# Kernel optimization log

Measured on AMD Instinct MI355X. Metric: run time of the kernel, lower is better.

## Reference

```python
import jax, jax.numpy as jnp
import numpy as np
import math

H, D = 8, 16
O = H * D  # out_channels = 128
N_TYPES = 2
EDGE_META = [(0, 1), (1, 0)]  # (src_type, dst_type) per edge type: user->item, item->user

def _segment_softmax(alpha, dst, n):
    # PyG softmax over incoming edges grouped by destination node
    amax = jax.ops.segment_max(alpha, dst, num_segments=n)
    amax = jnp.where(jnp.isfinite(amax), amax, 0.0)
    ex = jnp.exp(alpha - amax[dst])
    den = jax.ops.segment_sum(ex, dst, num_segments=n)
    return ex / (den[dst] + 1e-16)

def setup_inputs():
    key = jax.random.key(0)
    ks = jax.random.split(key, 8)
    N, E, I = 50000, 500000, 128
    s = 1.0 / math.sqrt(I)
    sd = 1.0 / math.sqrt(D)
    return {
        "x": jax.random.normal(ks[0], (N_TYPES, N, I), jnp.float32),
        "k_w": jax.random.normal(ks[1], (N_TYPES, O, I), jnp.float32) * s,
        "k_b": jnp.zeros((N_TYPES, O), jnp.float32),
        "q_w": jax.random.normal(ks[2], (N_TYPES, O, I), jnp.float32) * s,
        "q_b": jnp.zeros((N_TYPES, O), jnp.float32),
        "v_w": jax.random.normal(ks[3], (N_TYPES, O, I), jnp.float32) * s,
        "v_b": jnp.zeros((N_TYPES, O), jnp.float32),
        "a_w": jax.random.normal(ks[4], (N_TYPES, O, O), jnp.float32) * s,
        "a_b": jnp.zeros((N_TYPES, O), jnp.float32),
        "skip": jnp.ones((N_TYPES,), jnp.float32),
        "a_rel": jax.random.normal(ks[5], (2, H, D, D), jnp.float32) * sd,
        "m_rel": jax.random.normal(ks[6], (2, H, D, D), jnp.float32) * sd,
        "p_rel": jnp.ones((2, H), jnp.float32),
        "ln_g": jnp.ones((O,), jnp.float32),
        "ln_b": jnp.zeros((O,), jnp.float32),
        "edge_index": jax.random.randint(ks[7], (2, 2, E), 0, N, jnp.int32),
    }

def reference(x, k_w, k_b, q_w, q_b, v_w, v_b, a_w, a_b, skip, a_rel, m_rel, p_rel, ln_g, ln_b, edge_index):
    N = x.shape[1]
    lin = lambda xi, w, b: xi @ w.T + b
    # per-node-type K/Q/V projections -> [T, N, H, D]
    k = jnp.stack([lin(x[t], k_w[t], k_b[t]) for t in range(N_TYPES)]).reshape(N_TYPES, N, H, D)
    q = jnp.stack([lin(x[t], q_w[t], q_b[t]) for t in range(N_TYPES)]).reshape(N_TYPES, N, H, D)
    v = jnp.stack([lin(x[t], v_w[t], v_b[t]) for t in range(N_TYPES)]).reshape(N_TYPES, N, H, D)
    agg = jnp.zeros((N_TYPES, N, O), x.dtype)
    for e, (st, dt) in enumerate(EDGE_META):
        src, dst = edge_index[e, 0], edge_index[e, 1]
        ke = jnp.einsum('nhd,hde->nhe', k[st], a_rel[e])  # relation-transformed keys
        ve = jnp.einsum('nhd,hde->nhe', v[st], m_rel[e])  # relation-transformed values
        alpha = jnp.einsum('ehd,ehd->eh', q[dt][dst], ke[src]) * p_rel[e] / math.sqrt(D)
        alpha = _segment_softmax(alpha, dst, N)  # [E, H]
        msg = (ve[src] * alpha[..., None]).reshape(-1, O)
        agg = agg.at[dt].add(jax.ops.segment_sum(msg, dst, num_segments=N))
    outs = []
    for t in range(N_TYPES):
        o = lin(jax.nn.gelu(agg[t], approximate=False), a_w[t], a_b[t])
        beta = jax.nn.sigmoid(skip[t])
        o = beta * o + (1.0 - beta) * x[t]  # HGT skip (out_channels == in_channels)
        o = jax.nn.relu(o)
        mu = jnp.mean(o, axis=-1, keepdims=True)
        var = jnp.mean((o - mu) ** 2, axis=-1, keepdims=True)
        o = (o - mu) / jnp.sqrt(var + 1e-5) * ln_g + ln_b  # LayerNorm; dropout = identity (eval)
        outs.append(o)
    return jnp.stack(outs)  # [2, N, 128]
```

## Files before the change

kernel.cpp:

```cpp
#include <hip/hip_runtime.h>
#include <math.h>


#define EB_STRIDE 40

typedef __attribute__((ext_vector_type(8))) short short8;
typedef __attribute__((ext_vector_type(4))) float floatx4;

__device__ __forceinline__ float bf2f(unsigned int bits16) {
  union { unsigned int i; float f; } u; u.i = bits16 << 16; return u.f;
}
__device__ __forceinline__ float bf2f_hi(unsigned int u) {
  union { unsigned int i; float f; } v; v.i = u & 0xffff0000u; return v.f;
}
__device__ __forceinline__ unsigned short f2bf(float f) {
  union { float ff; unsigned int i; } u; u.ff = f;
  unsigned int x = u.i;
  x += 0x7fffu + ((x >> 16) & 1u);
  return (unsigned short)(x >> 16);
}

__global__ void fuse_weights(
    const float* __restrict__ k_w, const float* __restrict__ k_b,
    const float* __restrict__ q_w, const float* __restrict__ q_b,
    const float* __restrict__ v_w, const float* __restrict__ v_b,
    const float* __restrict__ a_w, const float* __restrict__ a_b,
    const float* __restrict__ a_rel, const float* __restrict__ m_rel,
    const float* __restrict__ p_rel,
    unsigned short* __restrict__ Wfb, float* __restrict__ Bf,
    int* __restrict__ cnt, int nC)
{
  int tid = blockIdx.x * 256 + threadIdx.x;
  if (tid < nC) cnt[tid] = 0;
  if (tid >= 2 * 4 * 128 * 128) return;
  int t   = tid >> 16;
  int rem = tid & 65535;
  int m   = rem >> 14;
  int o   = (rem >> 7) & 127;
  int i   = rem & 127;
  float w, bias;
  if (m == 0) {
    w    = q_w[t * 16384 + o * 128 + i];
    bias = q_b[t * 128 + o];
  } else if (m == 3) {
    w    = a_w[t * 16384 + o * 128 + i];
    bias = a_b[t * 128 + o];
  } else {
    const float* bw  = (m == 1) ? k_w : v_w;
    const float* bb  = (m == 1) ? k_b : v_b;
    const float* rel = (m == 1) ? a_rel : m_rel;
    int h = o >> 4, eo = o & 15;
    float s = 0.f, sb = 0.f;
    #pragma unroll
    for (int d = 0; d < 16; ++d) {
      float r = rel[t * 2048 + h * 256 + d * 16 + eo];
      s  += bw[t * 16384 + (h * 16 + d) * 128 + i] * r;
      sb += bb[t * 128 + h * 16 + d] * r;
    }
    if (m == 1) {
      float sc = p_rel[t * 8 + h] * 0.25f;
      s *= sc; sb *= sc;
    }
    w = s; bias = sb;
  }
  Wfb[tid] = f2bf(w);
  if (i == 0) Bf[t * 512 + m * 128 + o] = bias;
}

__global__ __launch_bounds__(256) void qkv_fill(
    const float* __restrict__ x, const unsigned short* __restrict__ Wfb,
    const float* __restrict__ Bf, unsigned short* __restrict__ qbuf,
    unsigned short* __restrict__ kvbuf,
    const int* __restrict__ ei, int* __restrict__ cnt, int* __restrict__ ebuf,
    int Nn, int E, int Gg)
{
  __shared__ alignas(16) unsigned short Als[64][136];
  __shared__ alignas(16) unsigned short Bls[128][136];
  const int b = blockIdx.x;
  const int tid = threadIdx.x;

  if (b >= Gg) {
    int f = b - Gg;
    int e = f & 1;
    int i = (f >> 1) * 256 + tid;
    if (i < E) {
      int src = ei[(size_t)e * 2 * E + i];
      int dst = ei[(size_t)e * 2 * E + E + i];
      int bk = (1 - e) * Nn + dst;
      int pos = atomicAdd(&cnt[bk], 1);
      if (pos < EB_STRIDE) ebuf[(size_t)bk * EB_STRIDE + pos] = src;
    }
    return;
  }

  const int t = b & 1;
  const int m0 = (b >> 1) * 64;
  const int lane = tid & 63, w = tid >> 6;
  const int col = lane & 15, quad = lane >> 4;
  const int morder[3] = {1, 2, 0};

  {
    int r = tid & 63, h = tid >> 6;
    int gn = m0 + r;
    if (gn < Nn) {
      const float* ap = x + (size_t)t * Nn * 128 + (size_t)gn * 128 + h * 32;
      #pragma unroll
      for (int j = 0; j < 8; ++j) {
        float4 f = ((const float4*)ap)[j];
        ushort4 s;
        s.x = f2bf(f.x); s.y = f2bf(f.y); s.z = f2bf(f.z); s.w = f2bf(f.w);
        *(ushort4*)&Als[r][h * 32 + j * 4] = s;
      }
    } else {
      ushort4 z = make_ushort4(0, 0, 0, 0);
      #pragma unroll
      for (int j = 0; j < 8; ++j) *(ushort4*)&Als[r][h * 32 + j * 4] = z;
    }
  }

  float acc_k[8][4];
  float bias_n[8];

  for (int mi_ = 0; mi_ < 3; ++mi_) {
    int m = morder[mi_];
    __syncthreads();
    {
      int r = tid & 127, h = tid >> 7;
      const unsigned short* wp = Wfb + (((size_t)(t * 4 + m)) << 14) + r * 128 + h * 64;
      #pragma unroll
      for (int j = 0; j < 8; ++j)
        *(uint4*)&Bls[r][h * 64 + j * 8] = ((const uint4*)wp)[j];
    }
    __syncthreads();

    floatx4 acc[8];
    #pragma unroll
    for (int ni = 0; ni < 8; ++ni) acc[ni] = (floatx4)(0.f);

    #pragma unroll
    for (int k0 = 0; k0 < 128; k0 += 32) {
      int kk = k0 + quad * 8;
      short8 a0 = *(const short8*)&Als[w * 16 + col][kk];
      #pragma unroll
      for (int ni = 0; ni < 8; ++ni) {
        short8 bb = *(const short8*)&Bls[ni * 16 + col][kk];
        acc[ni] = __builtin_amdgcn_mfma_f32_16x16x32_bf16(a0, bb, acc[ni], 0, 0, 0);
      }
    }

    const float* Bv = Bf + t * 512 + m * 128;
    #pragma unroll
    for (int ni = 0; ni < 8; ++ni) bias_n[ni] = Bv[ni * 16 + col];

    if (m == 1) {
      #pragma unroll
      for (int ni = 0; ni < 8; ++ni)
        #pragma unroll
        for (int reg = 0; reg < 4; ++reg)
          acc_k[ni][reg] = acc[ni][reg] + bias_n[ni];
    } else if (m == 2) {
      unsigned int* kvp = (unsigned int*)kvbuf + ((size_t)t * Nn) * 128;
      #pragma unroll
      for (int reg = 0; reg < 4; ++reg) {
        int row = m0 + w * 16 + quad * 4 + reg;
        if (row >= Nn) continue;
        unsigned int* cp = kvp + (size_t)row * 128 + col;
        #pragma unroll
        for (int ni = 0; ni < 8; ++ni) {
          unsigned int kbits = f2bf(acc_k[ni][reg]);
          unsigned int vbits = f2bf(acc[ni][reg] + bias_n[ni]);
          cp[ni * 16] = (vbits << 16) | kbits;
        }
      }
    } else {
      #pragma unroll
      for (int reg = 0; reg < 4; ++reg) {
        int row = m0 + w * 16 + quad * 4 + reg;
        if (row >= Nn) continue;
        unsigned short* cp = qbuf + ((size_t)t * Nn + row) * 128 + col;
        #pragma unroll
        for (int ni = 0; ni < 8; ++ni)
          cp[ni * 16] = f2bf(acc[ni][reg] + bias_n[ni]);
      }
    }
  }
}

__global__ __launch_bounds__(256) void gather_fused(
    const unsigned short* __restrict__ qbuf, const unsigned short* __restrict__ kvbuf,
    const int* __restrict__ cnt, const int* __restrict__ ebuf,
    unsigned short* __restrict__ gbuf, int N)
{
  int wid = (blockIdx.x * 256 + threadIdx.x) >> 6;
  int l = threadIdx.x & 63;
  if (wid >= 2 * N) return;
  int dt = (wid >= N) ? 1 : 0;
  int e  = 1 - dt;
  int deg = cnt[wid]; if (deg > EB_STRIDE) deg = EB_STRIDE;
  int g = l >> 4, gl = l & 15;

  uint4 qr = *(const uint4*)(qbuf + (size_t)wid * 128 + 8 * gl);
  float qv[8];
  qv[0] = bf2f(qr.x & 0xffffu); qv[1] = bf2f(qr.x >> 16);
  qv[2] = bf2f(qr.y & 0xffffu); qv[3] = bf2f(qr.y >> 16);
  qv[4] = bf2f(qr.z & 0xffffu); qv[5] = bf2f(qr.z >> 16);
  qv[6] = bf2f(qr.w & 0xffffu); qv[7] = bf2f(qr.w >> 16);

  const unsigned short* kvbase = kvbuf + ((size_t)e * N) * 256;
  const int* eb = ebuf + (size_t)wid * EB_STRIDE;
  int mysrc = (l < deg) ? eb[l] : 0;

  float acc[8];
  #pragma unroll
  for (int c = 0; c < 8; ++c) acc[c] = 0.f;
  float den = 0.f;

  for (int j0 = 0; j0 < deg; j0 += 4) {
    int j = j0 + g;
    bool valid = j < deg;
    int src = __shfl(mysrc, valid ? j : 0, 64);
    const unsigned short* kv = kvbase + (size_t)src * 256 + 16 * gl;
    uint4 a = *(const uint4*)kv;
    uint4 b = *(const uint4*)(kv + 8);
    float p;
    p = qv[0] * bf2f(a.x & 0xffffu);
    p = fmaf(qv[1], bf2f(a.y & 0xffffu), p);
    p = fmaf(qv[2], bf2f(a.z & 0xffffu), p);
    p = fmaf(qv[3], bf2f(a.w & 0xffffu), p);
    p = fmaf(qv[4], bf2f(b.x & 0xffffu), p);
    p = fmaf(qv[5], bf2f(b.y & 0xffffu), p);
    p = fmaf(qv[6], bf2f(b.z & 0xffffu), p);
    p = fmaf(qv[7], bf2f(b.w & 0xffffu), p);
    float pt = p + __shfl_xor(p, 1, 64);
    float ex = valid ? __expf(pt) : 0.f;
    den += ex;
    acc[0] = fmaf(ex, bf2f_hi(a.x), acc[0]);
    acc[1] = fmaf(ex, bf2f_hi(a.y), acc[1]);
    acc[2] = fmaf(ex, bf2f_hi(a.z), acc[2]);
    acc[3] = fmaf(ex, bf2f_hi(a.w), acc[3]);
    acc[4] = fmaf(ex, bf2f_hi(b.x), acc[4]);
    acc[5] = fmaf(ex, bf2f_hi(b.y), acc[5]);
    acc[6] = fmaf(ex, bf2f_hi(b.z), acc[6]);
    acc[7] = fmaf(ex, bf2f_hi(b.w), acc[7]);
  }

  #pragma unroll
  for (int off = 16; off < 64; off <<= 1) {
    #pragma unroll
    for (int c = 0; c < 8; ++c) acc[c] += __shfl_xor(acc[c], off, 64);
    den += __shfl_xor(den, off, 64);
  }

  if (g == 0) {
    float rden = 1.f / (den + 1e-16f);
    unsigned short r[8];
    #pragma unroll
    for (int c = 0; c < 8; ++c) {
      float gg = acc[c] * rden;
      r[c] = f2bf(0.5f * gg * (1.f + erff(gg * 0.70710678118654752f)));
    }
    unsigned short* op = gbuf + (size_t)wid * 128 + 8 * gl;
    *(ushort4*)op       = make_ushort4(r[0], r[1], r[2], r[3]);
    *(ushort4*)(op + 4) = make_ushort4(r[4], r[5], r[6], r[7]);
  }
}

__global__ __launch_bounds__(256) void gemm_ln(
    const unsigned short* __restrict__ gbuf, const unsigned short* __restrict__ Wfb,
    const float* __restrict__ Bf, const float* __restrict__ x,
    const float* __restrict__ skip, const float* __restrict__ ln_g,
    const float* __restrict__ ln_b, float* __restrict__ outp, int Nn)
{
  __shared__ alignas(16) unsigned short Als[64][136];
  __shared__ alignas(16) unsigned short Bls[128][136];
  const int tid = threadIdx.x;
  const int t = blockIdx.x & 1;
  const int m0 = (blockIdx.x >> 1) * 64;
  const int lane = tid & 63, w = tid >> 6;
  const int col = lane & 15, quad = lane >> 4;

  {
    int r = tid & 63, h = tid >> 6;
    int gn = m0 + r;
    if (gn < Nn) {
      const unsigned short* ap = gbuf + (size_t)t * Nn * 128 + (size_t)gn * 128 + h * 32;
      #pragma unroll
      for (int j = 0; j < 4; ++j)
        *(uint4*)&Als[r][h * 32 + j * 8] = ((const uint4*)ap)[j];
    } else {
      uint4 z = make_uint4(0, 0, 0, 0);
      #pragma unroll
      for (int j = 0; j < 4; ++j) *(uint4*)&Als[r][h * 32 + j * 8] = z;
    }
  }
  {
    int r = tid & 127, h = tid >> 7;
    const unsigned short* wp = Wfb + (((size_t)(t * 4 + 3)) << 14) + r * 128 + h * 64;
    #pragma unroll
    for (int j = 0; j < 8; ++j)
      *(uint4*)&Bls[r][h * 64 + j * 8] = ((const uint4*)wp)[j];
  }
  __syncthreads();

  floatx4 acc[8];
  #pragma unroll
  for (int ni = 0; ni < 8; ++ni) acc[ni] = (floatx4)(0.f);

  #pragma unroll
  for (int k0 = 0; k0 < 128; k0 += 32) {
    int kk = k0 + quad * 8;
    short8 a0 = *(const short8*)&Als[w * 16 + col][kk];
    #pragma unroll
    for (int ni = 0; ni < 8; ++ni) {
      short8 bb = *(const short8*)&Bls[ni * 16 + col][kk];
      acc[ni] = __builtin_amdgcn_mfma_f32_16x16x32_bf16(a0, bb, acc[ni], 0, 0, 0);
    }
  }

  const float* Bv = Bf + t * 512 + 3 * 128;
  float bias_n[8], g_n[8], b_n[8];
  #pragma unroll
  for (int ni = 0; ni < 8; ++ni) {
    bias_n[ni] = Bv[ni * 16 + col];
    g_n[ni]    = ln_g[ni * 16 + col];
    b_n[ni]    = ln_b[ni * 16 + col];
  }
  float sv = skip[t];
  float beta = 1.f / (1.f + __expf(-sv));
  const float* xt = x + (size_t)t * Nn * 128;
  float* op = outp + (size_t)t * Nn * 128;

  #pragma unroll
  for (int reg = 0; reg < 4; ++reg) {
    int row = m0 + w * 16 + quad * 4 + reg;
    if (row >= Nn) continue;
    const float* xr = xt + (size_t)row * 128;
    float vals[8], s = 0.f;
    #pragma unroll
    for (int ni = 0; ni < 8; ++ni) {
      float o = acc[ni][reg] + bias_n[ni];
      float v = fmaxf(beta * o + (1.f - beta) * xr[ni * 16 + col], 0.f);
      vals[ni] = v; s += v;
    }
    #pragma unroll
    for (int off = 1; off < 16; off <<= 1) s += __shfl_xor(s, off, 64);
    float mu = s * 0.0078125f;
    float sq = 0.f;
    #pragma unroll
    for (int ni = 0; ni < 8; ++ni) { float d = vals[ni] - mu; sq += d * d; }
    #pragma unroll
    for (int off = 1; off < 16; off <<= 1) sq += __shfl_xor(sq, off, 64);
    float rstd = rsqrtf(sq * 0.0078125f + 1e-5f);
    float* orow = op + (size_t)row * 128 + col;
    #pragma unroll
    for (int ni = 0; ni < 8; ++ni)
      orow[ni * 16] = (vals[ni] - mu) * rstd * g_n[ni] + b_n[ni];
  }
}

extern "C" void kernel_launch(void* const* d_in, const int* in_sizes, int n_in,
                              void* d_out, int out_size, void* d_ws, size_t ws_size,
                              hipStream_t stream) {
  const float* x     = (const float*)d_in[0];
  const float* k_w   = (const float*)d_in[1];
  const float* k_b   = (const float*)d_in[2];
  const float* q_w   = (const float*)d_in[3];
  const float* q_b   = (const float*)d_in[4];
  const float* v_w   = (const float*)d_in[5];
  const float* v_b   = (const float*)d_in[6];
  const float* a_w   = (const float*)d_in[7];
  const float* a_b   = (const float*)d_in[8];
  const float* skip  = (const float*)d_in[9];
  const float* a_rel = (const float*)d_in[10];
  const float* m_rel = (const float*)d_in[11];
  const float* p_rel = (const float*)d_in[12];
  const float* ln_g  = (const float*)d_in[13];
  const float* ln_b  = (const float*)d_in[14];
  const int* ei      = (const int*)d_in[15];
  float* out         = (float*)d_out;

  const int N = in_sizes[0] / 256;
  const int E = in_sizes[15] / 4;

  unsigned short* Wfb = (unsigned short*)d_ws;
  float* Bf = (float*)(Wfb + 2 * 4 * 128 * 128);
  unsigned short* qbuf = (unsigned short*)(Bf + 2 * 4 * 128);
  unsigned short* kvbuf = qbuf + (size_t)2 * N * 128;
  int* cnt  = (int*)(kvbuf + (size_t)2 * N * 256);
  int* ebuf = cnt + (size_t)2 * N;
  unsigned short* gbuf = (unsigned short*)(ebuf + (size_t)2 * N * EB_STRIDE);

  fuse_weights<<<(2 * 4 * 128 * 128 + 255) / 256, 256, 0, stream>>>(
      k_w, k_b, q_w, q_b, v_w, v_b, a_w, a_b, a_rel, m_rel, p_rel, Wfb, Bf,
      cnt, 2 * N);

  int Mb64 = (N + 63) / 64;
  int Gg = Mb64 * 2;
  int Fb = 2 * ((E + 255) / 256);
  qkv_fill<<<Gg + Fb, 256, 0, stream>>>(
      x, Wfb, Bf, qbuf, kvbuf, ei, cnt, ebuf, N, E, Gg);

  gather_fused<<<(2 * N * 64 + 255) / 256, 256, 0, stream>>>(
      qbuf, kvbuf, cnt, ebuf, gbuf, N);

  gemm_ln<<<Gg, 256, 0, stream>>>(
      gbuf, Wfb, Bf, x, skip, ln_g, ln_b, out, N);
}
```

Before: 301.8 us.

## Use 128-row tiles, XOR-swizzled LDS and direct global-to-LDS loads in GEMMs

Both MFMA GEMM kernels (the QKV projection and the output projection with LayerNorm) now process 128 rows per block, two 16-row fragments per wave, so each B-fragment read from LDS feeds two MFMAs. The padded LDS arrays are replaced with an XOR-swizzled layout that avoids bank conflicts. To match it, the fused weights and the gathered activations are written to global memory already swizzled, so tiles can be copied with global_load_lds straight into LDS without staging through registers. The cost is more accumulator registers per thread, possibly lower occupancy, and reads past the end of the activation buffer on the last tile.

```diff
diff --git a/kernel.cpp b/kernel.cpp
--- a/kernel.cpp
+++ b/kernel.cpp
@@ -13,11 +13,21 @@
 __device__ __forceinline__ float bf2f_hi(unsigned int u) {
   union { unsigned int i; float f; } v; v.i = u & 0xffff0000u; return v.f;
 }
-__device__ __forceinline__ unsigned short f2bf(float f) {
+__device__ __forceinline__ unsigned int f2bf(float f) {
   union { float ff; unsigned int i; } u; u.ff = f;
   unsigned int x = u.i;
   x += 0x7fffu + ((x >> 16) & 1u);
-  return (unsigned short)(x >> 16);
+  return x >> 16;
+}
+
+__device__ __forceinline__ void gld16(void* lds, const void* g) {
+  __builtin_amdgcn_global_load_lds(
+      (const __attribute__((address_space(1))) void*)g,
+      (__attribute__((address_space(3))) void*)lds, 16, 0, 0);
+}
+
+__device__ __forceinline__ short8 lds_frag(const unsigned short* base, int row, int g) {
+  return *(const short8*)&base[row * 128 + ((g ^ (row & 7)) << 3)];
 }
 
 __global__ void fuse_weights(
@@ -63,7 +73,8 @@
     }
     w = s; bias = sb;
   }
-  Wfb[tid] = f2bf(w);
+  int sidx = ((tid >> 7) << 7) | ((((i >> 3) ^ (o & 7)) << 3) | (i & 7));
+  Wfb[sidx] = (unsigned short)f2bf(w);
   if (i == 0) Bf[t * 512 + m * 128 + o] = bias;
 }
 
@@ -74,8 +85,8 @@
     const int* __restrict__ ei, int* __restrict__ cnt, int* __restrict__ ebuf,
     int Nn, int E, int Gg)
 {
-  __shared__ alignas(16) unsigned short Als[64][136];
-  __shared__ alignas(16) unsigned short Bls[128][136];
+  __shared__ alignas(16) unsigned short Als[16384];
+  __shared__ alignas(16) unsigned short Bls[16384];
   const int b = blockIdx.x;
   const int tid = threadIdx.x;
 
@@ -94,57 +105,70 @@
   }
 
   const int t = b & 1;
-  const int m0 = (b >> 1) * 64;
+  const int m0 = (b >> 1) * 128;
   const int lane = tid & 63, w = tid >> 6;
   const int col = lane & 15, quad = lane >> 4;
   const int morder[3] = {1, 2, 0};
 
   {
-    int r = tid & 63, h = tid >> 6;
+    int r = tid & 127, h = tid >> 7;
     int gn = m0 + r;
     if (gn < Nn) {
-      const float* ap = x + (size_t)t * Nn * 128 + (size_t)gn * 128 + h * 32;
+      const float* xrow = x + ((size_t)t * Nn + gn) * 128;
       #pragma unroll
       for (int j = 0; j < 8; ++j) {
-        float4 f = ((const float4*)ap)[j];
-        ushort4 s;
-        s.x = f2bf(f.x); s.y = f2bf(f.y); s.z = f2bf(f.z); s.w = f2bf(f.w);
-        *(ushort4*)&Als[r][h * 32 + j * 4] = s;
+        int g = h * 8 + j;
+        float4 f0 = *(const float4*)(xrow + g * 8);
+        float4 f1 = *(const float4*)(xrow + g * 8 + 4);
+        uint4 u;
+        u.x = f2bf(f0.x) | (f2bf(f0.y) << 16);
+        u.y = f2bf(f0.z) | (f2bf(f0.w) << 16);
+        u.z = f2bf(f1.x) | (f2bf(f1.y) << 16);
+        u.w = f2bf(f1.z) | (f2bf(f1.w) << 16);
+        *(uint4*)&Als[r * 128 + ((g ^ (r & 7)) << 3)] = u;
       }
     } else {
-      ushort4 z = make_ushort4(0, 0, 0, 0);
-      #pragma unroll
-      for (int j = 0; j < 8; ++j) *(ushort4*)&Als[r][h * 32 + j * 4] = z;
-    }
-  }
-
-  float acc_k[8][4];
+      uint4 z = make_uint4(0, 0, 0, 0);
+      #pragma unroll
+      for (int j = 0; j < 8; ++j) {
+        int g = h * 8 + j;
+        *(uint4*)&Als[r * 128 + ((g ^ (r & 7)) << 3)] = z;
+      }
+    }
+  }
+
+  float acc_k[2][8][4];
   float bias_n[8];
 
   for (int mi_ = 0; mi_ < 3; ++mi_) {
     int m = morder[mi_];
     __syncthreads();
     {
-      int r = tid & 127, h = tid >> 7;
-      const unsigned short* wp = Wfb + (((size_t)(t * 4 + m)) << 14) + r * 128 + h * 64;
-      #pragma unroll
-      for (int j = 0; j < 8; ++j)
-        *(uint4*)&Bls[r][h * 64 + j * 8] = ((const uint4*)wp)[j];
+      const unsigned short* Bm = Wfb + (((size_t)(t * 4 + m)) << 14);
+      #pragma unroll
+      for (int i = 0; i < 8; ++i) {
+        int cc = w * 8 + i;
+        gld16(&Bls[cc * 512], Bm + cc * 512 + lane * 8);
+      }
     }
     __syncthreads();
 
-    floatx4 acc[8];
-    #pragma unroll
-    for (int ni = 0; ni < 8; ++ni) acc[ni] = (floatx4)(0.f);
+    floatx4 acc[2][8];
+    #pragma unroll
+    for (int mi = 0; mi < 2; ++mi)
+      #pragma unroll
+      for (int ni = 0; ni < 8; ++ni) acc[mi][ni] = (floatx4)(0.f);
 
     #pragma unroll
     for (int k0 = 0; k0 < 128; k0 += 32) {
-      int kk = k0 + quad * 8;
-      short8 a0 = *(const short8*)&Als[w * 16 + col][kk];
+      int gk = (k0 >> 3) + quad;
+      short8 a0 = lds_frag(Als, w * 32 + col, gk);
+      short8 a1 = lds_frag(Als, w * 32 + 16 + col, gk);
       #pragma unroll
       for (int ni = 0; ni < 8; ++ni) {
-        short8 bb = *(const short8*)&Bls[ni * 16 + col][kk];
-        acc[ni] = __builtin_amdgcn_mfma_f32_16x16x32_bf16(a0, bb, acc[ni], 0, 0, 0);
+        short8 bf_ = lds_frag(Bls, ni * 16 + col, gk);
+        acc[0][ni] = __builtin_amdgcn_mfma_f32_16x16x32_bf16(a0, bf_, acc[0][ni], 0, 0, 0);
+        acc[1][ni] = __builtin_amdgcn_mfma_f32_16x16x32_bf16(a1, bf_, acc[1][ni], 0, 0, 0);
       }
     }
 
@@ -154,34 +178,40 @@
 
     if (m == 1) {
       #pragma unroll
-      for (int ni = 0; ni < 8; ++ni)
+      for (int mi = 0; mi < 2; ++mi)
         #pragma unroll
-        for (int reg = 0; reg < 4; ++reg)
-          acc_k[ni][reg] = acc[ni][reg] + bias_n[ni];
+        for (int ni = 0; ni < 8; ++ni)
+          #pragma unroll
+          for (int reg = 0; reg < 4; ++reg)
+            acc_k[mi][ni][reg] = acc[mi][ni][reg] + bias_n[ni];
     } else if (m == 2) {
       unsigned int* kvp = (unsigned int*)kvbuf + ((size_t)t * Nn) * 128;
       #pragma unroll
-      for (int reg = 0; reg < 4; ++reg) {
-        int row = m0 + w * 16 + quad * 4 + reg;
-        if (row >= Nn) continue;
-        unsigned int* cp = kvp + (size_t)row * 128 + col;
+      for (int mi = 0; mi < 2; ++mi)
         #pragma unroll
-        for (int ni = 0; ni < 8; ++ni) {
-          unsigned int kbits = f2bf(acc_k[ni][reg]);
-          unsigned int vbits = f2bf(acc[ni][reg] + bias_n[ni]);
-          cp[ni * 16] = (vbits << 16) | kbits;
+        for (int reg = 0; reg < 4; ++reg) {
+          int row = m0 + w * 32 + mi * 16 + quad * 4 + reg;
+          if (row >= Nn) continue;
+          unsigned int* cp = kvp + (size_t)row * 128 + col;
+          #pragma unroll
+          for (int ni = 0; ni < 8; ++ni) {
+            unsigned int kbits = f2bf(acc_k[mi][ni][reg]);
+            unsigned int vbits = f2bf(acc[mi][ni][reg] + bias_n[ni]);
+            cp[ni * 16] = (vbits << 16) | kbits;
+          }
         }
-      }
     } else {
       #pragma unroll
-      for (int reg = 0; reg < 4; ++reg) {
-        int row = m0 + w * 16 + quad * 4 + reg;
-        if (row >= Nn) continue;
-        unsigned short* cp = qbuf + ((size_t)t * Nn + row) * 128 + col;
+      for (int mi = 0; mi < 2; ++mi)
         #pragma unroll
-        for (int ni = 0; ni < 8; ++ni)
-          cp[ni * 16] = f2bf(acc[ni][reg] + bias_n[ni]);
-      }
+        for (int reg = 0; reg < 4; ++reg) {
+          int row = m0 + w * 32 + mi * 16 + quad * 4 + reg;
+          if (row >= Nn) continue;
+          unsigned short* cp = qbuf + ((size_t)t * Nn + row) * 128 + col;
+          #pragma unroll
+          for (int ni = 0; ni < 8; ++ni)
+            cp[ni * 16] = (unsigned short)f2bf(acc[mi][ni][reg] + bias_n[ni]);
+        }
     }
   }
 }
@@ -253,15 +283,16 @@
 
   if (g == 0) {
     float rden = 1.f / (den + 1e-16f);
-    unsigned short r[8];
+    unsigned int r[8];
     #pragma unroll
     for (int c = 0; c < 8; ++c) {
       float gg = acc[c] * rden;
       r[c] = f2bf(0.5f * gg * (1.f + erff(gg * 0.70710678118654752f)));
     }
-    unsigned short* op = gbuf + (size_t)wid * 128 + 8 * gl;
-    *(ushort4*)op       = make_ushort4(r[0], r[1], r[2], r[3]);
-    *(ushort4*)(op + 4) = make_ushort4(r[4], r[5], r[6], r[7]);
+    uint4 u;
+    u.x = r[0] | (r[1] << 16); u.y = r[2] | (r[3] << 16);
+    u.z = r[4] | (r[5] << 16); u.w = r[6] | (r[7] << 16);
+    *(uint4*)(gbuf + (size_t)wid * 128 + ((gl ^ (wid & 7)) << 3)) = u;
   }
 }
 
@@ -271,49 +302,42 @@
     const float* __restrict__ skip, const float* __restrict__ ln_g,
     const float* __restrict__ ln_b, float* __restrict__ outp, int Nn)
 {
-  __shared__ alignas(16) unsigned short Als[64][136];
-  __shared__ alignas(16) unsigned short Bls[128][136];
+  __shared__ alignas(16) unsigned short Als[16384];
+  __shared__ alignas(16) unsigned short Bls[16384];
   const int tid = threadIdx.x;
   const int t = blockIdx.x & 1;
-  const int m0 = (blockIdx.x >> 1) * 64;
+  const int m0 = (blockIdx.x >> 1) * 128;
   const int lane = tid & 63, w = tid >> 6;
   const int col = lane & 15, quad = lane >> 4;
 
   {
-    int r = tid & 63, h = tid >> 6;
-    int gn = m0 + r;
-    if (gn < Nn) {
-      const unsigned short* ap = gbuf + (size_t)t * Nn * 128 + (size_t)gn * 128 + h * 32;
-      #pragma unroll
-      for (int j = 0; j < 4; ++j)
-        *(uint4*)&Als[r][h * 32 + j * 8] = ((const uint4*)ap)[j];
-    } else {
-      uint4 z = make_uint4(0, 0, 0, 0);
-      #pragma unroll
-      for (int j = 0; j < 4; ++j) *(uint4*)&Als[r][h * 32 + j * 8] = z;
-    }
-  }
-  {
-    int r = tid & 127, h = tid >> 7;
-    const unsigned short* wp = Wfb + (((size_t)(t * 4 + 3)) << 14) + r * 128 + h * 64;
-    #pragma unroll
-    for (int j = 0; j < 8; ++j)
-      *(uint4*)&Bls[r][h * 64 + j * 8] = ((const uint4*)wp)[j];
+    const unsigned short* Ab = gbuf + ((size_t)t * Nn + m0) * 128;
+    const unsigned short* Bm = Wfb + (((size_t)(t * 4 + 3)) << 14);
+    #pragma unroll
+    for (int i = 0; i < 8; ++i) {
+      int cc = w * 8 + i;
+      gld16(&Als[cc * 512], Ab + (size_t)cc * 512 + lane * 8);
+      gld16(&Bls[cc * 512], Bm + cc * 512 + lane * 8);
+    }
   }
   __syncthreads();
 
-  floatx4 acc[8];
-  #pragma unroll
-  for (int ni = 0; ni < 8; ++ni) acc[ni] = (floatx4)(0.f);
+  floatx4 acc[2][8];
+  #pragma unroll
+  for (int mi = 0; mi < 2; ++mi)
+    #pragma unroll
+    for (int ni = 0; ni < 8; ++ni) acc[mi][ni] = (floatx4)(0.f);
 
   #pragma unroll
   for (int k0 = 0; k0 < 128; k0 += 32) {
-    int kk = k0 + quad * 8;
-    short8 a0 = *(const short8*)&Als[w * 16 + col][kk];
+    int gk = (k0 >> 3) + quad;
+    short8 a0 = lds_frag(Als, w * 32 + col, gk);
+    short8 a1 = lds_frag(Als, w * 32 + 16 + col, gk);
     #pragma unroll
     for (int ni = 0; ni < 8; ++ni) {
-      short8 bb = *(const short8*)&Bls[ni * 16 + col][kk];
-      acc[ni] = __builtin_amdgcn_mfma_f32_16x16x32_bf16(a0, bb, acc[ni], 0, 0, 0);
+      short8 bf_ = lds_frag(Bls, ni * 16 + col, gk);
+      acc[0][ni] = __builtin_amdgcn_mfma_f32_16x16x32_bf16(a0, bf_, acc[0][ni], 0, 0, 0);
+      acc[1][ni] = __builtin_amdgcn_mfma_f32_16x16x32_bf16(a1, bf_, acc[1][ni], 0, 0, 0);
     }
   }
 
@@ -331,31 +355,33 @@
   float* op = outp + (size_t)t * Nn * 128;
 
   #pragma unroll
-  for (int reg = 0; reg < 4; ++reg) {
-    int row = m0 + w * 16 + quad * 4 + reg;
-    if (row >= Nn) continue;
-    const float* xr = xt + (size_t)row * 128;
-    float vals[8], s = 0.f;
-    #pragma unroll
-    for (int ni = 0; ni < 8; ++ni) {
-      float o = acc[ni][reg] + bias_n[ni];
-      float v = fmaxf(beta * o + (1.f - beta) * xr[ni * 16 + col], 0.f);
-      vals[ni] = v; s += v;
-    }
-    #pragma unroll
-    for (int off = 1; off < 16; off <<= 1) s += __shfl_xor(s, off, 64);
-    float mu = s * 0.0078125f;
-    float sq = 0.f;
-    #pragma unroll
-    for (int ni = 0; ni < 8; ++ni) { float d = vals[ni] - mu; sq += d * d; }
-    #pragma unroll
-    for (int off = 1; off < 16; off <<= 1) sq += __shfl_xor(sq, off, 64);
-    float rstd = rsqrtf(sq * 0.0078125f + 1e-5f);
-    float* orow = op + (size_t)row * 128 + col;
-    #pragma unroll
-    for (int ni = 0; ni < 8; ++ni)
-      orow[ni * 16] = (vals[ni] - mu) * rstd * g_n[ni] + b_n[ni];
-  }
+  for (int mi = 0; mi < 2; ++mi)
+    #pragma unroll
+    for (int reg = 0; reg < 4; ++reg) {
+      int row = m0 + w * 32 + mi * 16 + quad * 4 + reg;
+      if (row >= Nn) continue;
+      const float* xr = xt + (size_t)row * 128;
+      float vals[8], s = 0.f;
+      #pragma unroll
+      for (int ni = 0; ni < 8; ++ni) {
+        float o = acc[mi][ni][reg] + bias_n[ni];
+        float v = fmaxf(beta * o + (1.f - beta) * xr[ni * 16 + col], 0.f);
+        vals[ni] = v; s += v;
+      }
+      #pragma unroll
+      for (int off = 1; off < 16; off <<= 1) s += __shfl_xor(s, off, 64);
+      float mu = s * 0.0078125f;
+      float sq = 0.f;
+      #pragma unroll
+      for (int ni = 0; ni < 8; ++ni) { float d = vals[ni] - mu; sq += d * d; }
+      #pragma unroll
+      for (int off = 1; off < 16; off <<= 1) sq += __shfl_xor(sq, off, 64);
+      float rstd = rsqrtf(sq * 0.0078125f + 1e-5f);
+      float* orow = op + (size_t)row * 128 + col;
+      #pragma unroll
+      for (int ni = 0; ni < 8; ++ni)
+        orow[ni * 16] = (vals[ni] - mu) * rstd * g_n[ni] + b_n[ni];
+    }
 }
 
 extern "C" void kernel_launch(void* const* d_in, const int* in_sizes, int n_in,
@@ -394,8 +420,8 @@
       k_w, k_b, q_w, q_b, v_w, v_b, a_w, a_b, a_rel, m_rel, p_rel, Wfb, Bf,
       cnt, 2 * N);
 
-  int Mb64 = (N + 63) / 64;
-  int Gg = Mb64 * 2;
+  int Mb = (N + 127) / 128;
+  int Gg = Mb * 2;
   int Fb = 2 * ((E + 255) / 256);
   qkv_fill<<<Gg + Fb, 256, 0, stream>>>(
       x, Wfb, Bf, qbuf, kvbuf, ei, cnt, ebuf, N, E, Gg);
```

Result: no change. 302.0 us (+0.1%).

## Drop LDS staging in QKV and output GEMMs, load MFMA operands from global

Applied to the files above, without the earlier changes.

Both the QKV projection and the output GEMM+LayerNorm kernels stop staging A and B tiles in shared memory. They load MFMA operands directly from global memory, with weights expected to be served from cache. The QKV kernel now computes Q, K and V in a single pass with three accumulator sets instead of three sequential weight-tile loads separated by barriers. This removes LDS traffic, the barriers and the LDS footprint, which may raise occupancy. In exchange it uses more registers (96 accumulator floats) and issues uncoalesced 16-byte global loads per lane.

```diff
diff --git a/kernel.cpp b/kernel.cpp
--- a/kernel.cpp
+++ b/kernel.cpp
@@ -7,17 +7,19 @@
 typedef __attribute__((ext_vector_type(8))) short short8;
 typedef __attribute__((ext_vector_type(4))) float floatx4;
 
+union S8U { uint4 u; short8 s; };
+
 __device__ __forceinline__ float bf2f(unsigned int bits16) {
   union { unsigned int i; float f; } u; u.i = bits16 << 16; return u.f;
 }
 __device__ __forceinline__ float bf2f_hi(unsigned int u) {
   union { unsigned int i; float f; } v; v.i = u & 0xffff0000u; return v.f;
 }
-__device__ __forceinline__ unsigned short f2bf(float f) {
+__device__ __forceinline__ unsigned int f2bf(float f) {
   union { float ff; unsigned int i; } u; u.ff = f;
   unsigned int x = u.i;
   x += 0x7fffu + ((x >> 16) & 1u);
-  return (unsigned short)(x >> 16);
+  return x >> 16;
 }
 
 __global__ void fuse_weights(
@@ -63,7 +65,7 @@
     }
     w = s; bias = sb;
   }
-  Wfb[tid] = f2bf(w);
+  Wfb[tid] = (unsigned short)f2bf(w);
   if (i == 0) Bf[t * 512 + m * 128 + o] = bias;
 }
 
@@ -74,8 +76,6 @@
     const int* __restrict__ ei, int* __restrict__ cnt, int* __restrict__ ebuf,
     int Nn, int E, int Gg)
 {
-  __shared__ alignas(16) unsigned short Als[64][136];
-  __shared__ alignas(16) unsigned short Bls[128][136];
   const int b = blockIdx.x;
   const int tid = threadIdx.x;
 
@@ -97,91 +97,64 @@
   const int m0 = (b >> 1) * 64;
   const int lane = tid & 63, w = tid >> 6;
   const int col = lane & 15, quad = lane >> 4;
-  const int morder[3] = {1, 2, 0};
-
-  {
-    int r = tid & 63, h = tid >> 6;
-    int gn = m0 + r;
-    if (gn < Nn) {
-      const float* ap = x + (size_t)t * Nn * 128 + (size_t)gn * 128 + h * 32;
-      #pragma unroll
-      for (int j = 0; j < 8; ++j) {
-        float4 f = ((const float4*)ap)[j];
-        ushort4 s;
-        s.x = f2bf(f.x); s.y = f2bf(f.y); s.z = f2bf(f.z); s.w = f2bf(f.w);
-        *(ushort4*)&Als[r][h * 32 + j * 4] = s;
-      }
-    } else {
-      ushort4 z = make_ushort4(0, 0, 0, 0);
-      #pragma unroll
-      for (int j = 0; j < 8; ++j) *(ushort4*)&Als[r][h * 32 + j * 4] = z;
-    }
-  }
-
-  float acc_k[8][4];
-  float bias_n[8];
-
-  for (int mi_ = 0; mi_ < 3; ++mi_) {
-    int m = morder[mi_];
-    __syncthreads();
-    {
-      int r = tid & 127, h = tid >> 7;
-      const unsigned short* wp = Wfb + (((size_t)(t * 4 + m)) << 14) + r * 128 + h * 64;
-      #pragma unroll
-      for (int j = 0; j < 8; ++j)
-        *(uint4*)&Bls[r][h * 64 + j * 8] = ((const uint4*)wp)[j];
-    }
-    __syncthreads();
-
-    floatx4 acc[8];
-    #pragma unroll
-    for (int ni = 0; ni < 8; ++ni) acc[ni] = (floatx4)(0.f);
-
-    #pragma unroll
-    for (int k0 = 0; k0 < 128; k0 += 32) {
-      int kk = k0 + quad * 8;
-      short8 a0 = *(const short8*)&Als[w * 16 + col][kk];
-      #pragma unroll
-      for (int ni = 0; ni < 8; ++ni) {
-        short8 bb = *(const short8*)&Bls[ni * 16 + col][kk];
-        acc[ni] = __builtin_amdgcn_mfma_f32_16x16x32_bf16(a0, bb, acc[ni], 0, 0, 0);
-      }
-    }
-
-    const float* Bv = Bf + t * 512 + m * 128;
-    #pragma unroll
-    for (int ni = 0; ni < 8; ++ni) bias_n[ni] = Bv[ni * 16 + col];
-
-    if (m == 1) {
-      #pragma unroll
-      for (int ni = 0; ni < 8; ++ni)
-        #pragma unroll
-        for (int reg = 0; reg < 4; ++reg)
-          acc_k[ni][reg] = acc[ni][reg] + bias_n[ni];
-    } else if (m == 2) {
-      unsigned int* kvp = (unsigned int*)kvbuf + ((size_t)t * Nn) * 128;
-      #pragma unroll
-      for (int reg = 0; reg < 4; ++reg) {
-        int row = m0 + w * 16 + quad * 4 + reg;
-        if (row >= Nn) continue;
-        unsigned int* cp = kvp + (size_t)row * 128 + col;
-        #pragma unroll
-        for (int ni = 0; ni < 8; ++ni) {
-          unsigned int kbits = f2bf(acc_k[ni][reg]);
-          unsigned int vbits = f2bf(acc[ni][reg] + bias_n[ni]);
-          cp[ni * 16] = (vbits << 16) | kbits;
-        }
-      }
-    } else {
-      #pragma unroll
-      for (int reg = 0; reg < 4; ++reg) {
-        int row = m0 + w * 16 + quad * 4 + reg;
-        if (row >= Nn) continue;
-        unsigned short* cp = qbuf + ((size_t)t * Nn + row) * 128 + col;
-        #pragma unroll
-        for (int ni = 0; ni < 8; ++ni)
-          cp[ni * 16] = f2bf(acc[ni][reg] + bias_n[ni]);
-      }
+
+  int rA = m0 + w * 16 + col;
+  if (rA >= Nn) rA = Nn - 1;
+  const float* arow = x + ((size_t)t * Nn + rA) * 128;
+
+  const unsigned short* Wq = Wfb + (((size_t)(t * 4 + 0)) << 14);
+  const unsigned short* Wk = Wfb + (((size_t)(t * 4 + 1)) << 14);
+  const unsigned short* Wv = Wfb + (((size_t)(t * 4 + 2)) << 14);
+
+  floatx4 aq[8], ak[8], av[8];
+  #pragma unroll
+  for (int ni = 0; ni < 8; ++ni) {
+    aq[ni] = (floatx4)(0.f); ak[ni] = (floatx4)(0.f); av[ni] = (floatx4)(0.f);
+  }
+
+  #pragma unroll
+  for (int k0 = 0; k0 < 128; k0 += 32) {
+    int ko = k0 + quad * 8;
+    float4 f0 = *(const float4*)(arow + ko);
+    float4 f1 = *(const float4*)(arow + ko + 4);
+    S8U a;
+    a.u.x = f2bf(f0.x) | (f2bf(f0.y) << 16);
+    a.u.y = f2bf(f0.z) | (f2bf(f0.w) << 16);
+    a.u.z = f2bf(f1.x) | (f2bf(f1.y) << 16);
+    a.u.w = f2bf(f1.z) | (f2bf(f1.w) << 16);
+    #pragma unroll
+    for (int ni = 0; ni < 8; ++ni) {
+      size_t boff = (size_t)(ni * 16 + col) * 128 + ko;
+      short8 bq = *(const short8*)(Wq + boff);
+      short8 bk = *(const short8*)(Wk + boff);
+      short8 bv = *(const short8*)(Wv + boff);
+      aq[ni] = __builtin_amdgcn_mfma_f32_16x16x32_bf16(a.s, bq, aq[ni], 0, 0, 0);
+      ak[ni] = __builtin_amdgcn_mfma_f32_16x16x32_bf16(a.s, bk, ak[ni], 0, 0, 0);
+      av[ni] = __builtin_amdgcn_mfma_f32_16x16x32_bf16(a.s, bv, av[ni], 0, 0, 0);
+    }
+  }
+
+  float bq_n[8], bk_n[8], bv_n[8];
+  #pragma unroll
+  for (int ni = 0; ni < 8; ++ni) {
+    bq_n[ni] = Bf[t * 512 + 0 * 128 + ni * 16 + col];
+    bk_n[ni] = Bf[t * 512 + 1 * 128 + ni * 16 + col];
+    bv_n[ni] = Bf[t * 512 + 2 * 128 + ni * 16 + col];
+  }
+
+  unsigned int* kvp = (unsigned int*)kvbuf + ((size_t)t * Nn) * 128;
+  #pragma unroll
+  for (int reg = 0; reg < 4; ++reg) {
+    int row = m0 + w * 16 + quad * 4 + reg;
+    if (row >= Nn) continue;
+    unsigned short* qp = qbuf + ((size_t)t * Nn + row) * 128 + col;
+    unsigned int* cp = kvp + (size_t)row * 128 + col;
+    #pragma unroll
+    for (int ni = 0; ni < 8; ++ni) {
+      qp[ni * 16] = (unsigned short)f2bf(aq[ni][reg] + bq_n[ni]);
+      unsigned int kbits = f2bf(ak[ni][reg] + bk_n[ni]);
+      unsigned int vbits = f2bf(av[ni][reg] + bv_n[ni]);
+      cp[ni * 16] = (vbits << 16) | kbits;
     }
   }
 }
@@ -257,7 +230,7 @@
     #pragma unroll
     for (int c = 0; c < 8; ++c) {
       float gg = acc[c] * rden;
-      r[c] = f2bf(0.5f * gg * (1.f + erff(gg * 0.70710678118654752f)));
+      r[c] = (unsigned short)f2bf(0.5f * gg * (1.f + erff(gg * 0.70710678118654752f)));
     }
     unsigned short* op = gbuf + (size_t)wid * 128 + 8 * gl;
     *(ushort4*)op       = make_ushort4(r[0], r[1], r[2], r[3]);
@@ -271,36 +244,16 @@
     const float* __restrict__ skip, const float* __restrict__ ln_g,
     const float* __restrict__ ln_b, float* __restrict__ outp, int Nn)
 {
-  __shared__ alignas(16) unsigned short Als[64][136];
-  __shared__ alignas(16) unsigned short Bls[128][136];
   const int tid = threadIdx.x;
   const int t = blockIdx.x & 1;
   const int m0 = (blockIdx.x >> 1) * 64;
   const int lane = tid & 63, w = tid >> 6;
   const int col = lane & 15, quad = lane >> 4;
 
-  {
-    int r = tid & 63, h = tid >> 6;
-    int gn = m0 + r;
-    if (gn < Nn) {
-      const unsigned short* ap = gbuf + (size_t)t * Nn * 128 + (size_t)gn * 128 + h * 32;
-      #pragma unroll
-      for (int j = 0; j < 4; ++j)
-        *(uint4*)&Als[r][h * 32 + j * 8] = ((const uint4*)ap)[j];
-    } else {
-      uint4 z = make_uint4(0, 0, 0, 0);
-      #pragma unroll
-      for (int j = 0; j < 4; ++j) *(uint4*)&Als[r][h * 32 + j * 8] = z;
-    }
-  }
-  {
-    int r = tid & 127, h = tid >> 7;
-    const unsigned short* wp = Wfb + (((size_t)(t * 4 + 3)) << 14) + r * 128 + h * 64;
-    #pragma unroll
-    for (int j = 0; j < 8; ++j)
-      *(uint4*)&Bls[r][h * 64 + j * 8] = ((const uint4*)wp)[j];
-  }
-  __syncthreads();
+  int rA = m0 + w * 16 + col;
+  if (rA >= Nn) rA = Nn - 1;
+  const unsigned short* arow = gbuf + ((size_t)t * Nn + rA) * 128;
+  const unsigned short* Bm = Wfb + (((size_t)(t * 4 + 3)) << 14);
 
   floatx4 acc[8];
   #pragma unroll
@@ -308,12 +261,12 @@
 
   #pragma unroll
   for (int k0 = 0; k0 < 128; k0 += 32) {
-    int kk = k0 + quad * 8;
-    short8 a0 = *(const short8*)&Als[w * 16 + col][kk];
+    int ko = k0 + quad * 8;
+    short8 a = *(const short8*)(arow + ko);
     #pragma unroll
     for (int ni = 0; ni < 8; ++ni) {
-      short8 bb = *(const short8*)&Bls[ni * 16 + col][kk];
-      acc[ni] = __builtin_amdgcn_mfma_f32_16x16x32_bf16(a0, bb, acc[ni], 0, 0, 0);
+      short8 bb = *(const short8*)(Bm + (size_t)(ni * 16 + col) * 128 + ko);
+      acc[ni] = __builtin_amdgcn_mfma_f32_16x16x32_bf16(a, bb, acc[ni], 0, 0, 0);
     }
   }
 
@@ -394,8 +347,8 @@
       k_w, k_b, q_w, q_b, v_w, v_b, a_w, a_b, a_rel, m_rel, p_rel, Wfb, Bf,
       cnt, 2 * N);
 
-  int Mb64 = (N + 63) / 64;
-  int Gg = Mb64 * 2;
+  int Mb = (N + 63) / 64;
+  int Gg = Mb * 2;
   int Fb = 2 * ((E + 255) / 256);
   qkv_fill<<<Gg + Fb, 256, 0, stream>>>(
       x, Wfb, Bf, qbuf, kvbuf, ei, cnt, ebuf, N, E, Gg);
```

After: 350.5 us. 16.1% more time.
